# Kernel optimization log

Measured on AMD Instinct MI355X. Metric: run time of the kernel, lower is better.

The kernel has to match this reference:

```python
import jax, jax.numpy as jnp
import numpy as np

D_MODEL = 1024
D_STATE = 128
D_CONV = 4
EXPAND = 2
HEADDIM = 64
D_INNER = EXPAND * D_MODEL          # 2048
NHEADS = D_INNER // HEADDIM         # 32
NGROUPS = 1
CONV_DIM = D_INNER + 2 * NGROUPS * D_STATE            # 2304
D_IN_PROJ = 2 * D_INNER + 2 * NGROUPS * D_STATE + NHEADS  # 4384
NUM_CLASS = 48
BATCH = 2
SEQLEN = 512


def setup_inputs() -> dict:
    key = jax.random.key(0)
    ks = jax.random.split(key, 8)
    s = 0.02
    inputs = jax.random.normal(ks[0], (BATCH, SEQLEN, D_MODEL), jnp.float32)
    W_in = jax.random.normal(ks[1], (D_MODEL, D_IN_PROJ), jnp.float32) * s
    conv_w = jax.random.normal(ks[2], (CONV_DIM, D_CONV), jnp.float32) * 0.2
    conv_b = jnp.zeros((CONV_DIM,), jnp.float32)
    # dt_bias = inverse-softplus of dt sampled in [1e-3, 0.1] (mamba init)
    dt = jnp.exp(jax.random.uniform(ks[3], (NHEADS,), jnp.float32) * (np.log(0.1) - np.log(1e-3)) + np.log(1e-3))
    dt_bias = dt + jnp.log(-jnp.expm1(-dt))
    A_log = jnp.log(jax.random.uniform(ks[4], (NHEADS,), jnp.float32, 1.0, 16.0))
    D = jnp.ones((NHEADS,), jnp.float32)
    norm_w = jnp.ones((D_INNER,), jnp.float32)
    W_out = jax.random.normal(ks[5], (D_INNER, D_MODEL), jnp.float32) * s
    W_cls = jax.random.normal(ks[6], (D_INNER, NUM_CLASS), jnp.float32) * s
    b_cls = jnp.zeros((NUM_CLASS,), jnp.float32)
    return {"inputs": inputs, "W_in": W_in, "conv_w": conv_w, "conv_b": conv_b,
            "dt_bias": dt_bias, "A_log": A_log, "D": D, "norm_w": norm_w,
            "W_out": W_out, "W_cls": W_cls, "b_cls": b_cls}


def _forward(inputs, W_in, conv_w, conv_b, dt_bias, A_log, D, norm_w, W_out, W_cls, b_cls):
    B, L, _ = inputs.shape
    zxbcdt = inputs @ W_in                                     # (B,L,4384)
    z, xBC, dt = jnp.split(zxbcdt, [D_INNER, D_INNER + CONV_DIM], axis=-1)
    dt = jax.nn.softplus(dt + dt_bias)                         # (B,L,H)
    # causal depthwise conv over time on (x,B,C)
    xBC_t = jnp.pad(jnp.transpose(xBC, (0, 2, 1)), ((0, 0), (0, 0), (D_CONV - 1, 0)))
    xBC_c = jax.lax.conv_general_dilated(xBC_t, conv_w[:, None, :], (1,), 'VALID',
                                         feature_group_count=CONV_DIM)
    xBC = jax.nn.silu(jnp.transpose(xBC_c, (0, 2, 1)) + conv_b)
    x, Bm, Cm = jnp.split(xBC, [D_INNER, D_INNER + D_STATE], axis=-1)
    x = x.reshape(B, L, NHEADS, HEADDIM)
    A = -jnp.exp(A_log)                                        # (H,)
    dA = jnp.exp(dt * A)                                       # (B,L,H)

    def step(state, inp):
        # state: (B,H,P,N) -- selective SSM recurrence (chunk_size=1 path)
        x_t, B_t, C_t, dt_t, dA_t = inp
        state = state * dA_t[:, :, None, None] + jnp.einsum('bhp,bn,bh->bhpn', x_t, B_t, dt_t)
        y_t = jnp.einsum('bhpn,bn->bhp', state, C_t)
        return state, y_t

    state0 = jnp.zeros((B, NHEADS, HEADDIM, D_STATE), inputs.dtype)
    xs = (jnp.transpose(x, (1, 0, 2, 3)), jnp.transpose(Bm, (1, 0, 2)),
          jnp.transpose(Cm, (1, 0, 2)), jnp.transpose(dt, (1, 0, 2)),
          jnp.transpose(dA, (1, 0, 2)))
    _, ys = jax.lax.scan(step, state0, xs)                     # ys: (L,B,H,P)
    y = jnp.transpose(ys, (1, 0, 2, 3)) + D[None, None, :, None] * x
    y = y.reshape(B, L, D_INNER)
    # gated RMSNorm: rmsnorm(y * silu(z)) * weight
    y = y * jax.nn.silu(z)
    y = y * jax.lax.rsqrt(jnp.mean(y * y, axis=-1, keepdims=True) + 1e-5) * norm_w
    # hidden_states (d_inner=2048) go through the per-timestep classifier
    preds = y @ W_cls + b_cls                                  # (B,L,num_class)
    return preds


def reference(inputs, W_in, conv_w, conv_b, dt_bias, A_log, D, norm_w, W_out, W_cls, b_cls):
    return _forward(inputs, W_in, conv_w, conv_b, dt_bias, A_log, D, norm_w, W_out, W_cls, b_cls)
```

## Files before the change

### kernel.cpp

```cpp
#include <hip/hip_runtime.h>
#include <hip/hip_bf16.h>
#include <cstdint>

#define BATCH 2
#define SEQLEN 512
#define BL (BATCH*SEQLEN)
#define DMODEL 1024
#define DINNER 2048
#define NHEADS 32
#define HEADDIM 64
#define DSTATE 128
#define CONVDIM 2304
#define DINPROJ 4384
#define NPROJPAD 4480
#define NCLS 48
#define QC 64
#define NCH 8

typedef short bf16x8 __attribute__((ext_vector_type(8)));
typedef float f32x4  __attribute__((ext_vector_type(4)));
typedef unsigned int u32;
typedef const __attribute__((address_space(1))) u32 gu32;
typedef __attribute__((address_space(3))) u32 lu32;

static __device__ __forceinline__ void gl16(const void* g, void* l) {
    __builtin_amdgcn_global_load_lds((gu32*)g, (lu32*)l, 16, 0, 0);
}

static __device__ __forceinline__ unsigned short f2bf(float f) {
    unsigned u = __float_as_uint(f);
    unsigned r = (u + 0x7FFFu + ((u >> 16) & 1u)) >> 16;
    return (unsigned short)r;
}
static __device__ __forceinline__ float bf2f(unsigned short u) {
    return __uint_as_float(((unsigned)u) << 16);
}

__global__ __launch_bounds__(256) void k_prep(const float* __restrict__ in,
                                              unsigned short* __restrict__ abf,
                                              const float* __restrict__ W,
                                              unsigned short* __restrict__ Wt,
                                              const float* __restrict__ Wcls,
                                              unsigned short* __restrict__ Wtc) {
    __shared__ float tile[32][33];
    int bid = blockIdx.x;
    int tid = threadIdx.x;
    if (bid < 1024) {
        int i = (bid * 256 + tid) * 4;
        float4 v = *(const float4*)(in + i);
        ushort4 o;
        o.x = f2bf(v.x); o.y = f2bf(v.y); o.z = f2bf(v.z); o.w = f2bf(v.w);
        *(ushort4*)(abf + i) = o;
    } else if (bid < 1024 + 4384) {
        int t = bid - 1024;
        int n0 = (t % 137) * 32;
        int k0 = (t / 137) * 32;
        int tx = tid & 31, ty = tid >> 5;
#pragma unroll
        for (int i = 0; i < 4; ++i) {
            int k = k0 + ty + i * 8;
            tile[ty + i * 8][tx] = W[(size_t)k * DINPROJ + n0 + tx];
        }
        __syncthreads();
#pragma unroll
        for (int i = 0; i < 4; ++i) {
            int n = n0 + ty + i * 8;
            Wt[(size_t)n * DMODEL + k0 + tx] = f2bf(tile[tx][ty + i * 8]);
        }
    } else {
        int n = bid - (1024 + 4384);
        for (int k = tid; k < DINNER; k += 256)
            Wtc[(size_t)n * DINNER + k] = f2bf(Wcls[(size_t)k * NCLS + n]);
    }
}

__global__ __launch_bounds__(256) void k_gemm_in(const unsigned short* __restrict__ A,
                                                 const unsigned short* __restrict__ Bt,
                                                 unsigned short* __restrict__ C) {
    __shared__ unsigned short As[2 * 4096];
    __shared__ unsigned short Bs[2 * 5120];
    const int tid  = threadIdx.x;
    const int m0   = blockIdx.y * 128;
    const int n0   = blockIdx.x * 160;
    const int w    = tid >> 6;
    const int lane = tid & 63;
    const int wm   = w >> 1, wn = w & 1;
    const int fr   = lane & 15, fq = lane >> 4;
    const int lrow = lane >> 2;
    const int skg  = (lane & 3) * 8;
    const unsigned short* gA0 = A + (size_t)(m0 + w * 16 + lrow) * DMODEL + skg;
    const unsigned short* gA1 = gA0 + (size_t)64 * DMODEL;

    f32x4 acc[4][5] = {};
    for (int k0 = 0; k0 < DMODEL; k0 += 64) {
        __syncthreads();
#pragma unroll
        for (int hh = 0; hh < 2; ++hh) {
            int kg = k0 + hh * 32;
            gl16(gA0 + kg, As + hh * 4096 + w * 512);
            gl16(gA1 + kg, As + hh * 4096 + 2048 + w * 512);
            for (int o = w; o < 10; o += 4) {
                const unsigned short* gB = Bt + (size_t)(n0 + o * 16 + lrow) * DMODEL + skg + kg;
                gl16(gB, Bs + hh * 5120 + o * 512);
            }
        }
        __syncthreads();
#pragma unroll
        for (int hh = 0; hh < 2; ++hh) {
            bf16x8 af[4], bfr[5];
#pragma unroll
            for (int mt = 0; mt < 4; ++mt)
                af[mt] = *(const bf16x8*)(&As[hh * 4096 + (wm * 64 + mt * 16 + fr) * 32 + fq * 8]);
#pragma unroll
            for (int nt = 0; nt < 5; ++nt)
                bfr[nt] = *(const bf16x8*)(&Bs[hh * 5120 + (wn * 80 + nt * 16 + fr) * 32 + fq * 8]);
#pragma unroll
            for (int mt = 0; mt < 4; ++mt)
#pragma unroll
                for (int nt = 0; nt < 5; ++nt)
                    acc[mt][nt] = __builtin_amdgcn_mfma_f32_16x16x32_bf16(af[mt], bfr[nt], acc[mt][nt], 0, 0, 0);
        }
    }
#pragma unroll
    for (int mt = 0; mt < 4; ++mt) {
#pragma unroll
        for (int nt = 0; nt < 5; ++nt) {
            int col = n0 + wn * 80 + nt * 16 + fr;
            if (col < DINPROJ) {
#pragma unroll
                for (int r = 0; r < 4; ++r) {
                    int row = m0 + wm * 64 + mt * 16 + fq * 4 + r;
                    C[(size_t)row * DINPROJ + col] = f2bf(acc[mt][nt][r]);
                }
            }
        }
    }
}

__global__ __launch_bounds__(256) void k_conv_dt(const unsigned short* __restrict__ zx,
                                                 const float* __restrict__ conv_w,
                                                 const float* __restrict__ conv_b,
                                                 const float* __restrict__ dt_bias,
                                                 float* __restrict__ xbc,
                                                 float* __restrict__ dtb) {
    int row = blockIdx.y;
    int c   = blockIdx.x * 256 + threadIdx.x;
    int b = row >> 9, l = row & 511;
    if (c < CONVDIM) {
        float acc = conv_b[c];
#pragma unroll
        for (int j = 0; j < 4; ++j) {
            int ls = l - 3 + j;
            float v = (ls >= 0) ? bf2f(zx[((size_t)(b * SEQLEN + ls)) * DINPROJ + DINNER + c]) : 0.f;
            acc += v * conv_w[c * 4 + j];
        }
        float s = acc / (1.f + expf(-acc));
        xbc[(size_t)row * CONVDIM + c] = s;
    } else if (c < CONVDIM + NHEADS) {
        int h = c - CONVDIM;
        float raw = bf2f(zx[(size_t)row * DINPROJ + (DINNER + CONVDIM) + h]) + dt_bias[h];
        float dt = (raw > 20.f) ? raw : log1pf(expf(raw));
        dtb[row * NHEADS + h] = dt;
    }
}

__global__ __launch_bounds__(256) void k_chunk(const float* __restrict__ xbc,
                                               const float* __restrict__ dtb,
                                               const float* __restrict__ A_log,
                                               const float* __restrict__ Dvec,
                                               unsigned short* __restrict__ yb,
                                               unsigned short* __restrict__ Sc_bf,
                                               float* __restrict__ lam_g,
                                               float* __restrict__ esc_g) {
    const int gid = blockIdx.x;
    const int cq = gid & 7;
    const int h = (gid >> 3) & 31;
    const int b = gid >> 8;
    const int row0 = b * SEQLEN + cq * QC;

    __shared__ float cumS[QC], wS[QC], dtS[QC];
    __shared__ unsigned short Xt[QC][72];
    __shared__ unsigned short Bs[QC][136];
    __shared__ unsigned short BtW[DSTATE][72];
    __shared__ unsigned short Cs[QC][136];
    __shared__ unsigned short Gs[QC][72];

    const int tid = threadIdx.x;
    if (tid < 64) {
        float dtv = dtb[(size_t)(row0 + tid) * NHEADS + h];
        float nA = -expf(A_log[h]);
        float x = dtv * nA;
#pragma unroll
        for (int off = 1; off < 64; off <<= 1) {
            float v = __shfl_up(x, off, 64);
            if (tid >= off) x += v;
        }
        float cumTot = __shfl(x, 63, 64);
        cumS[tid] = x;
        dtS[tid] = dtv;
        wS[tid] = expf(cumTot - x) * dtv;
        esc_g[(size_t)gid * QC + tid] = expf(x);
        if (tid == 0) lam_g[gid] = expf(cumTot);
    }
    __syncthreads();

    {
        int row = tid >> 2;
        int g = tid & 3;
        const float* rp = xbc + (size_t)(row0 + row) * CONVDIM;
        float wrow = wS[row];
#pragma unroll
        for (int i = 0; i < 4; ++i) {
            float4 v = *(const float4*)(rp + h * HEADDIM + g * 16 + i * 4);
            int p = g * 16 + i * 4;
            Xt[p + 0][row] = f2bf(v.x);
            Xt[p + 1][row] = f2bf(v.y);
            Xt[p + 2][row] = f2bf(v.z);
            Xt[p + 3][row] = f2bf(v.w);
        }
#pragma unroll
        for (int i = 0; i < 8; ++i) {
            int n = g * 32 + i * 4;
            float4 v = *(const float4*)(rp + DINNER + n);
            ushort4 u;
            u.x = f2bf(v.x); u.y = f2bf(v.y); u.z = f2bf(v.z); u.w = f2bf(v.w);
            *(ushort4*)(&Bs[row][n]) = u;
            BtW[n + 0][row] = f2bf(v.x * wrow);
            BtW[n + 1][row] = f2bf(v.y * wrow);
            BtW[n + 2][row] = f2bf(v.z * wrow);
            BtW[n + 3][row] = f2bf(v.w * wrow);
        }
#pragma unroll
        for (int i = 0; i < 8; ++i) {
            int n = g * 32 + i * 4;
            float4 v = *(const float4*)(rp + DINNER + DSTATE + n);
            ushort4 u;
            u.x = f2bf(v.x); u.y = f2bf(v.y); u.z = f2bf(v.z); u.w = f2bf(v.w);
            *(ushort4*)(&Cs[row][n]) = u;
        }
    }
    __syncthreads();

    const int w = tid >> 6, lane = tid & 63;
    const int fr = lane & 15, fq = lane >> 4, fk = (lane >> 4) * 8;

    f32x4 accG[4] = {};
#pragma unroll
    for (int kk = 0; kk < 4; ++kk) {
        bf16x8 a = *(const bf16x8*)(&Cs[w * 16 + fr][kk * 32 + fk]);
#pragma unroll
        for (int nt = 0; nt < 4; ++nt) {
            bf16x8 bb = *(const bf16x8*)(&Bs[nt * 16 + fr][kk * 32 + fk]);
            accG[nt] = __builtin_amdgcn_mfma_f32_16x16x32_bf16(a, bb, accG[nt], 0, 0, 0);
        }
    }
#pragma unroll
    for (int nt = 0; nt < 4; ++nt) {
        int s = nt * 16 + fr;
        float cs = cumS[s], dts = dtS[s];
#pragma unroll
        for (int r = 0; r < 4; ++r) {
            int t = w * 16 + fq * 4 + r;
            float val = (s <= t) ? accG[nt][r] * expf(cumS[t] - cs) * dts : 0.f;
            Gs[t][s] = f2bf(val);
        }
    }
    __syncthreads();

    f32x4 accY[4] = {};
#pragma unroll
    for (int kk = 0; kk < 2; ++kk) {
        bf16x8 a = *(const bf16x8*)(&Gs[w * 16 + fr][kk * 32 + fk]);
#pragma unroll
        for (int pt = 0; pt < 4; ++pt) {
            bf16x8 bb = *(const bf16x8*)(&Xt[pt * 16 + fr][kk * 32 + fk]);
            accY[pt] = __builtin_amdgcn_mfma_f32_16x16x32_bf16(a, bb, accY[pt], 0, 0, 0);
        }
    }
    f32x4 accS[8] = {};
#pragma unroll
    for (int kk = 0; kk < 2; ++kk) {
        bf16x8 a = *(const bf16x8*)(&Xt[w * 16 + fr][kk * 32 + fk]);
#pragma unroll
        for (int nt = 0; nt < 8; ++nt) {
            bf16x8 bb = *(const bf16x8*)(&BtW[nt * 16 + fr][kk * 32 + fk]);
            accS[nt] = __builtin_amdgcn_mfma_f32_16x16x32_bf16(a, bb, accS[nt], 0, 0, 0);
        }
    }
    float Dh = Dvec[h];
#pragma unroll
    for (int pt = 0; pt < 4; ++pt) {
        int p = pt * 16 + fr;
#pragma unroll
        for (int r = 0; r < 4; ++r) {
            int t = w * 16 + fq * 4 + r;
            float xv = bf2f(Xt[p][t]);
            yb[(size_t)(row0 + t) * DINNER + h * HEADDIM + p] = f2bf(accY[pt][r] + Dh * xv);
        }
    }
    unsigned short* scp = Sc_bf + (size_t)gid * (HEADDIM * DSTATE);
#pragma unroll
    for (int nt = 0; nt < 8; ++nt) {
        int n = nt * 16 + fr;
#pragma unroll
        for (int r = 0; r < 4; ++r) {
            int p = w * 16 + fq * 4 + r;
            scp[p * DSTATE + n] = f2bf(accS[nt][r]);
        }
    }
}

__global__ __launch_bounds__(256) void k_chain(const unsigned short* __restrict__ Sc_bf,
                                               const float* __restrict__ lam_g,
                                               unsigned short* __restrict__ Sin_bf) {
    int bh = blockIdx.x >> 2;
    int sl = blockIdx.x & 3;
    int tid = threadIdx.x;
    float s[8];
#pragma unroll
    for (int i = 0; i < 8; ++i) s[i] = 0.f;
    for (int c = 0; c < NCH; ++c) {
        size_t base = (size_t)(bh * NCH + c) * (HEADDIM * DSTATE) + sl * 2048 + tid * 8;
        ushort4 o0, o1;
        o0.x = f2bf(s[0]); o0.y = f2bf(s[1]); o0.z = f2bf(s[2]); o0.w = f2bf(s[3]);
        o1.x = f2bf(s[4]); o1.y = f2bf(s[5]); o1.z = f2bf(s[6]); o1.w = f2bf(s[7]);
        *(ushort4*)(Sin_bf + base) = o0;
        *(ushort4*)(Sin_bf + base + 4) = o1;
        float lam = lam_g[bh * NCH + c];
        ushort4 v0 = *(const ushort4*)(Sc_bf + base);
        ushort4 v1 = *(const ushort4*)(Sc_bf + base + 4);
        s[0] = s[0] * lam + bf2f(v0.x);
        s[1] = s[1] * lam + bf2f(v0.y);
        s[2] = s[2] * lam + bf2f(v0.z);
        s[3] = s[3] * lam + bf2f(v0.w);
        s[4] = s[4] * lam + bf2f(v1.x);
        s[5] = s[5] * lam + bf2f(v1.y);
        s[6] = s[6] * lam + bf2f(v1.z);
        s[7] = s[7] * lam + bf2f(v1.w);
    }
}

__global__ __launch_bounds__(256) void k_cross(const float* __restrict__ xbc,
                                               const float* __restrict__ esc_g,
                                               const unsigned short* __restrict__ Sin_bf,
                                               unsigned short* __restrict__ yb) {
    const int gid = blockIdx.x;
    const int cq = gid & 7;
    const int h = (gid >> 3) & 31;
    const int b = gid >> 8;
    const int row0 = b * SEQLEN + cq * QC;
    __shared__ unsigned short Ct[QC][136];
    __shared__ unsigned short Ss[QC][136];
    const int tid = threadIdx.x;
    {
        int row = tid >> 2, g = tid & 3;
        const float* rp = xbc + (size_t)(row0 + row) * CONVDIM + DINNER + DSTATE;
        float esc = esc_g[(size_t)gid * QC + row];
#pragma unroll
        for (int i = 0; i < 8; ++i) {
            int n = g * 32 + i * 4;
            float4 v = *(const float4*)(rp + n);
            ushort4 u;
            u.x = f2bf(v.x * esc); u.y = f2bf(v.y * esc);
            u.z = f2bf(v.z * esc); u.w = f2bf(v.w * esc);
            *(ushort4*)(&Ct[row][n]) = u;
        }
        const uint4* sp = (const uint4*)(Sin_bf + (size_t)gid * (HEADDIM * DSTATE));
#pragma unroll
        for (int i = 0; i < 4; ++i) {
            uint4 v = sp[row * 16 + g * 4 + i];
            *(uint4*)(&Ss[row][g * 32 + i * 8]) = v;
        }
    }
    __syncthreads();
    const int w = tid >> 6, lane = tid & 63;
    const int fr = lane & 15, fq = lane >> 4, fk = (lane >> 4) * 8;
    f32x4 acc[4] = {};
#pragma unroll
    for (int kk = 0; kk < 4; ++kk) {
        bf16x8 a = *(const bf16x8*)(&Ct[w * 16 + fr][kk * 32 + fk]);
#pragma unroll
        for (int pt = 0; pt < 4; ++pt) {
            bf16x8 bb = *(const bf16x8*)(&Ss[pt * 16 + fr][kk * 32 + fk]);
            acc[pt] = __builtin_amdgcn_mfma_f32_16x16x32_bf16(a, bb, acc[pt], 0, 0, 0);
        }
    }
#pragma unroll
    for (int pt = 0; pt < 4; ++pt) {
        int p = pt * 16 + fr;
#pragma unroll
        for (int r = 0; r < 4; ++r) {
            int t = w * 16 + fq * 4 + r;
            size_t yi = (size_t)(row0 + t) * DINNER + h * HEADDIM + p;
            yb[yi] = f2bf(bf2f(yb[yi]) + acc[pt][r]);
        }
    }
}

__global__ __launch_bounds__(256) void k_gn_cls(const unsigned short* __restrict__ zx,
                                                const unsigned short* __restrict__ yb,
                                                const float* __restrict__ nw,
                                                const unsigned short* __restrict__ Wt,
                                                const float* __restrict__ bcls,
                                                float* __restrict__ out) {
    __shared__ unsigned short Gs[16][2048];
    __shared__ float scaleS[16];
    __shared__ float Rs[3][4][256];
    const int m0 = blockIdx.x * 16;
    const int tid = threadIdx.x;
    const int w = tid >> 6, lane = tid & 63;

#pragma unroll
    for (int i = 0; i < 4; ++i) {
        int rl = w * 4 + i;
        int row = m0 + rl;
        const unsigned short* yr = yb + (size_t)row * DINNER;
        const unsigned short* zr = zx + (size_t)row * DINPROJ;
        float gv[32];
        float ss = 0.f;
#pragma unroll
        for (int i2 = 0; i2 < 4; ++i2) {
            int k = i2 * 512 + lane * 8;
            ushort4 ya = *(const ushort4*)(yr + k);
            ushort4 ybq = *(const ushort4*)(yr + k + 4);
            ushort4 za = *(const ushort4*)(zr + k);
            ushort4 zbq = *(const ushort4*)(zr + k + 4);
            float ys[8] = {bf2f(ya.x), bf2f(ya.y), bf2f(ya.z), bf2f(ya.w),
                           bf2f(ybq.x), bf2f(ybq.y), bf2f(ybq.z), bf2f(ybq.w)};
            float zs[8] = {bf2f(za.x), bf2f(za.y), bf2f(za.z), bf2f(za.w),
                           bf2f(zbq.x), bf2f(zbq.y), bf2f(zbq.z), bf2f(zbq.w)};
#pragma unroll
            for (int j = 0; j < 8; ++j) {
                float sil = zs[j] / (1.f + expf(-zs[j]));
                float gg = ys[j] * sil;
                gv[i2 * 8 + j] = gg;
                ss += gg * gg;
            }
        }
#pragma unroll
        for (int off = 32; off >= 1; off >>= 1) ss += __shfl_xor(ss, off, 64);
        if (lane == 0) scaleS[rl] = rsqrtf(ss / (float)DINNER + 1e-5f);
#pragma unroll
        for (int i2 = 0; i2 < 4; ++i2) {
            int k = i2 * 512 + lane * 8;
            ushort4 u0, u1;
            u0.x = f2bf(gv[i2 * 8 + 0]); u0.y = f2bf(gv[i2 * 8 + 1]);
            u0.z = f2bf(gv[i2 * 8 + 2]); u0.w = f2bf(gv[i2 * 8 + 3]);
            u1.x = f2bf(gv[i2 * 8 + 4]); u1.y = f2bf(gv[i2 * 8 + 5]);
            u1.z = f2bf(gv[i2 * 8 + 6]); u1.w = f2bf(gv[i2 * 8 + 7]);
            *(ushort4*)(&Gs[rl][k]) = u0;
            *(ushort4*)(&Gs[rl][k + 4]) = u1;
        }
    }
    __syncthreads();
    {
        int k0 = tid * 8;
        float4 n0 = *(const float4*)(nw + k0);
        float4 n1 = *(const float4*)(nw + k0 + 4);
        float nv[8] = {n0.x, n0.y, n0.z, n0.w, n1.x, n1.y, n1.z, n1.w};
#pragma unroll
        for (int r = 0; r < 16; ++r) {
            float sc = scaleS[r];
            ushort4 a0 = *(const ushort4*)(&Gs[r][k0]);
            ushort4 a1 = *(const ushort4*)(&Gs[r][k0 + 4]);
            ushort4 o0, o1;
            o0.x = f2bf(bf2f(a0.x) * sc * nv[0]); o0.y = f2bf(bf2f(a0.y) * sc * nv[1]);
            o0.z = f2bf(bf2f(a0.z) * sc * nv[2]); o0.w = f2bf(bf2f(a0.w) * sc * nv[3]);
            o1.x = f2bf(bf2f(a1.x) * sc * nv[4]); o1.y = f2bf(bf2f(a1.y) * sc * nv[5]);
            o1.z = f2bf(bf2f(a1.z) * sc * nv[6]); o1.w = f2bf(bf2f(a1.w) * sc * nv[7]);
            *(ushort4*)(&Gs[r][k0]) = o0;
            *(ushort4*)(&Gs[r][k0 + 4]) = o1;
        }
    }
    __syncthreads();
    const int fr = lane & 15, fq = lane >> 4;
    f32x4 acc[3] = {};
    const int kbase = w * 512;
    for (int ks = 0; ks < 16; ++ks) {
        int k0 = kbase + ks * 32;
        bf16x8 a = *(const bf16x8*)(&Gs[fr][k0 + fq * 8]);
#pragma unroll
        for (int nt = 0; nt < 3; ++nt) {
            bf16x8 bb = *(const bf16x8*)(Wt + (size_t)(nt * 16 + fr) * DINNER + k0 + fq * 8);
            acc[nt] = __builtin_amdgcn_mfma_f32_16x16x32_bf16(a, bb, acc[nt], 0, 0, 0);
        }
    }
#pragma unroll
    for (int nt = 0; nt < 3; ++nt)
        *(f32x4*)(&Rs[nt][w][lane * 4]) = acc[nt];
    __syncthreads();
    if (tid < 64) {
#pragma unroll
        for (int nt = 0; nt < 3; ++nt) {
            int col = nt * 16 + (lane & 15);
            float bb = bcls[col];
#pragma unroll
            for (int j = 0; j < 4; ++j) {
                float s = Rs[nt][0][lane * 4 + j] + Rs[nt][1][lane * 4 + j]
                        + Rs[nt][2][lane * 4 + j] + Rs[nt][3][lane * 4 + j];
                int row = m0 + (lane >> 4) * 4 + j;
                out[(size_t)row * NCLS + col] = s + bb;
            }
        }
    }
}

extern "C" void kernel_launch(void* const* d_in, const int* in_sizes, int n_in,
                              void* d_out, int out_size, void* d_ws, size_t ws_size,
                              hipStream_t stream) {
    const float* inputs  = (const float*)d_in[0];
    const float* W_in    = (const float*)d_in[1];
    const float* conv_w  = (const float*)d_in[2];
    const float* conv_b  = (const float*)d_in[3];
    const float* dt_bias = (const float*)d_in[4];
    const float* A_log   = (const float*)d_in[5];
    const float* Dvec    = (const float*)d_in[6];
    const float* norm_w  = (const float*)d_in[7];
    const float* W_cls   = (const float*)d_in[9];
    const float* b_cls   = (const float*)d_in[10];
    float* out = (float*)d_out;

    float* ws = (float*)d_ws;
    unsigned short* zxb = (unsigned short*)ws;
    float* xbc   = ws + (size_t)BL * DINPROJ / 2;
    float* dtb   = xbc + (size_t)BL * CONVDIM;
    float* lam_g = dtb + (size_t)BL * NHEADS;
    float* esc_g = lam_g + 512;
    unsigned short* yb     = (unsigned short*)(esc_g + 512 * QC);
    unsigned short* Sc_bf  = yb + (size_t)BL * DINNER;
    unsigned short* Sin_bf = Sc_bf + (size_t)512 * HEADDIM * DSTATE;
    unsigned short* abf    = Sin_bf + (size_t)512 * HEADDIM * DSTATE;
    unsigned short* wtbf   = abf + (size_t)BL * DMODEL;
    unsigned short* wclsbf = wtbf + (size_t)NPROJPAD * DMODEL;

    k_prep<<<dim3(1024 + 4384 + 48), dim3(256), 0, stream>>>(inputs, abf, W_in, wtbf,
                                                             W_cls, wclsbf);
    k_gemm_in<<<dim3(NPROJPAD / 160, BL / 128), dim3(256), 0, stream>>>(abf, wtbf, zxb);
    k_conv_dt<<<dim3(10, BL), dim3(256), 0, stream>>>(zxb, conv_w, conv_b, dt_bias, xbc, dtb);
    k_chunk<<<dim3(BATCH * NHEADS * NCH), dim3(256), 0, stream>>>(xbc, dtb, A_log, Dvec,
                                                                  yb, Sc_bf, lam_g, esc_g);
    k_chain<<<dim3(BATCH * NHEADS * 4), dim3(256), 0, stream>>>(Sc_bf, lam_g, Sin_bf);
    k_cross<<<dim3(BATCH * NHEADS * NCH), dim3(256), 0, stream>>>(xbc, esc_g, Sin_bf, yb);
    k_gn_cls<<<dim3(BL / 16), dim3(256), 0, stream>>>(zxb, yb, norm_w, wclsbf, b_cls, out);
}
```

Measured before the change: 172.1 us.

## Fuse inter-chunk state chain into cross kernel via weighted prefix sums

Removes the separate k_chain kernel that sequentially propagated chunk states. Each k_cross block now builds its own incoming state directly, as a decay-weighted sum of all earlier chunk states, using products of the lambda values. Chunk 0 blocks exit early. This saves one kernel launch and the Sin buffer round-trip. In exchange, total state reads grow quadratically with the chunk count, the summation is done in registers, and the rounding differs slightly from the old recurrence.

Result: no change. 174.7 us (+1.5%).

```diff
diff --git a/kernel.cpp b/kernel.cpp
--- a/kernel.cpp
+++ b/kernel.cpp
@@ -310,48 +310,30 @@
     }
 }
 
-__global__ __launch_bounds__(256) void k_chain(const unsigned short* __restrict__ Sc_bf,
-                                               const float* __restrict__ lam_g,
-                                               unsigned short* __restrict__ Sin_bf) {
-    int bh = blockIdx.x >> 2;
-    int sl = blockIdx.x & 3;
-    int tid = threadIdx.x;
-    float s[8];
-#pragma unroll
-    for (int i = 0; i < 8; ++i) s[i] = 0.f;
-    for (int c = 0; c < NCH; ++c) {
-        size_t base = (size_t)(bh * NCH + c) * (HEADDIM * DSTATE) + sl * 2048 + tid * 8;
-        ushort4 o0, o1;
-        o0.x = f2bf(s[0]); o0.y = f2bf(s[1]); o0.z = f2bf(s[2]); o0.w = f2bf(s[3]);
-        o1.x = f2bf(s[4]); o1.y = f2bf(s[5]); o1.z = f2bf(s[6]); o1.w = f2bf(s[7]);
-        *(ushort4*)(Sin_bf + base) = o0;
-        *(ushort4*)(Sin_bf + base + 4) = o1;
-        float lam = lam_g[bh * NCH + c];
-        ushort4 v0 = *(const ushort4*)(Sc_bf + base);
-        ushort4 v1 = *(const ushort4*)(Sc_bf + base + 4);
-        s[0] = s[0] * lam + bf2f(v0.x);
-        s[1] = s[1] * lam + bf2f(v0.y);
-        s[2] = s[2] * lam + bf2f(v0.z);
-        s[3] = s[3] * lam + bf2f(v0.w);
-        s[4] = s[4] * lam + bf2f(v1.x);
-        s[5] = s[5] * lam + bf2f(v1.y);
-        s[6] = s[6] * lam + bf2f(v1.z);
-        s[7] = s[7] * lam + bf2f(v1.w);
-    }
-}
-
 __global__ __launch_bounds__(256) void k_cross(const float* __restrict__ xbc,
                                                const float* __restrict__ esc_g,
-                                               const unsigned short* __restrict__ Sin_bf,
+                                               const unsigned short* __restrict__ Sc_bf,
+                                               const float* __restrict__ lam_g,
                                                unsigned short* __restrict__ yb) {
     const int gid = blockIdx.x;
     const int cq = gid & 7;
+    if (cq == 0) return;
     const int h = (gid >> 3) & 31;
     const int b = gid >> 8;
     const int row0 = b * SEQLEN + cq * QC;
     __shared__ unsigned short Ct[QC][136];
     __shared__ unsigned short Ss[QC][136];
     const int tid = threadIdx.x;
+    const int gbase = gid & ~7;
+
+    float coef[NCH - 1];
+    {
+        float prod = 1.f;
+        for (int c2 = cq - 1; c2 >= 0; --c2) {
+            coef[c2] = prod;
+            prod *= lam_g[gbase + c2];
+        }
+    }
     {
         int row = tid >> 2, g = tid & 3;
         const float* rp = xbc + (size_t)(row0 + row) * CONVDIM + DINNER + DSTATE;
@@ -365,11 +347,30 @@
             u.z = f2bf(v.z * esc); u.w = f2bf(v.w * esc);
             *(ushort4*)(&Ct[row][n]) = u;
         }
-        const uint4* sp = (const uint4*)(Sin_bf + (size_t)gid * (HEADDIM * DSTATE));
-#pragma unroll
-        for (int i = 0; i < 4; ++i) {
-            uint4 v = sp[row * 16 + g * 4 + i];
-            *(uint4*)(&Ss[row][g * 32 + i * 8]) = v;
+        float acc32[32];
+#pragma unroll
+        for (int i = 0; i < 32; ++i) acc32[i] = 0.f;
+        for (int c2 = 0; c2 < cq; ++c2) {
+            const unsigned short* sp = Sc_bf + (size_t)(gbase + c2) * (HEADDIM * DSTATE)
+                                     + row * DSTATE + g * 32;
+            float cf = coef[c2];
+#pragma unroll
+            for (int i = 0; i < 8; ++i) {
+                ushort4 v = *(const ushort4*)(sp + i * 4);
+                acc32[i * 4 + 0] += cf * bf2f(v.x);
+                acc32[i * 4 + 1] += cf * bf2f(v.y);
+                acc32[i * 4 + 2] += cf * bf2f(v.z);
+                acc32[i * 4 + 3] += cf * bf2f(v.w);
+            }
+        }
+#pragma unroll
+        for (int i = 0; i < 8; ++i) {
+            ushort4 u;
+            u.x = f2bf(acc32[i * 4 + 0]);
+            u.y = f2bf(acc32[i * 4 + 1]);
+            u.z = f2bf(acc32[i * 4 + 2]);
+            u.w = f2bf(acc32[i * 4 + 3]);
+            *(ushort4*)(&Ss[row][g * 32 + i * 4]) = u;
         }
     }
     __syncthreads();
@@ -528,8 +529,7 @@
     float* esc_g = lam_g + 512;
     unsigned short* yb     = (unsigned short*)(esc_g + 512 * QC);
     unsigned short* Sc_bf  = yb + (size_t)BL * DINNER;
-    unsigned short* Sin_bf = Sc_bf + (size_t)512 * HEADDIM * DSTATE;
-    unsigned short* abf    = Sin_bf + (size_t)512 * HEADDIM * DSTATE;
+    unsigned short* abf    = Sc_bf + (size_t)512 * HEADDIM * DSTATE;
     unsigned short* wtbf   = abf + (size_t)BL * DMODEL;
     unsigned short* wclsbf = wtbf + (size_t)NPROJPAD * DMODEL;
 
@@ -539,7 +539,7 @@
     k_conv_dt<<<dim3(10, BL), dim3(256), 0, stream>>>(zxb, conv_w, conv_b, dt_bias, xbc, dtb);
     k_chunk<<<dim3(BATCH * NHEADS * NCH), dim3(256), 0, stream>>>(xbc, dtb, A_log, Dvec,
                                                                   yb, Sc_bf, lam_g, esc_g);
-    k_chain<<<dim3(BATCH * NHEADS * 4), dim3(256), 0, stream>>>(Sc_bf, lam_g, Sin_bf);
-    k_cross<<<dim3(BATCH * NHEADS * NCH), dim3(256), 0, stream>>>(xbc, esc_g, Sin_bf, yb);
+    k_cross<<<dim3(BATCH * NHEADS * NCH), dim3(256), 0, stream>>>(xbc, esc_g, Sc_bf,
+                                                                  lam_g, yb);
     k_gn_cls<<<dim3(BL / 16), dim3(256), 0, stream>>>(zxb, yb, norm_w, wclsbf, b_cls, out);
 }
```
